# Kernel optimization log

Hardware: AMD Instinct MI355X
Metric: run time of the kernel (lower is better)

Reference implementation:

```python
import jax, jax.numpy as jnp
import numpy as np

B, C, W, H, K = 8, 512, 64, 64, 64
C4 = C // 4

def setup_inputs() -> dict:
    key = jax.random.key(0)
    ks = jax.random.split(key, 12)
    return {
        "x1": jax.random.normal(ks[0], (B, C, W, H), jnp.float32),
        "y1": jax.random.normal(ks[1], (B, K, C), jnp.float32),
        "x2": jax.random.normal(ks[2], (B, C, W, H), jnp.float32),
        "y2": jax.random.normal(ks[3], (B, K, C), jnp.float32),
        "wq": jax.random.normal(ks[4], (C4, C), jnp.float32) * 0.02,
        "bq": jax.random.normal(ks[5], (C4,), jnp.float32) * 0.02,
        "wk": jax.random.normal(ks[6], (C4, C), jnp.float32) * 0.02,
        "bk": jax.random.normal(ks[7], (C4,), jnp.float32) * 0.02,
        "wv": jax.random.normal(ks[8], (C, C), jnp.float32) * 0.02,
        "bv": jax.random.normal(ks[9], (C,), jnp.float32) * 0.02,
        "scale": jax.random.normal(ks[10], (1,), jnp.float32),
        "scale1": jax.random.normal(ks[11], (1,), jnp.float32),
    }

def reference(x1, y1, x2, y2, wq, bq, wk, bk, wv, bv, scale, scale1):
    b, c, w, h = x1.shape
    k = y1.shape[1]
    n = w * h
    # value projections (nn.Linear: y @ W^T + b), kept as [B, C, K]
    pv1 = jnp.einsum('bkc,dc->bdk', y1, wv) + bv[None, :, None]
    pv2 = jnp.einsum('bkc,dc->bdk', y2, wv) + bv[None, :, None]
    # 1x1 conv query: [B, C4, W, H] -> [B, N, C4]
    q = jnp.einsum('bcwh,dc->bwhd', x2, wq) + bq
    q = q.reshape(b, n, -1)
    # key: [B, K, C4] -> bmm contracts over C4
    kk = jnp.einsum('bkc,dc->bkd', y2, wk) + bk  # [B, K, C4]
    energy = jnp.einsum('bnd,bkd->bnk', q, kk)   # [B, N, K]
    attention = jax.nn.softmax(jnp.abs(energy), axis=-1)
    # out = value [B,C,K] @ attention^T [B,K,N] -> [B,C,N]
    out1 = jnp.einsum('bck,bnk->bcn', pv1, attention).reshape(b, c, w, h)
    out1 = scale[0] * out1 + x1
    out2 = jnp.einsum('bck,bnk->bcn', pv2, attention).reshape(b, c, w, h)
    out2 = scale1[0] * out2 + x2
    return (out1, out2)
```

## Files before the change

### kernel.cpp

```cpp
#include <hip/hip_runtime.h>
#include <math.h>

#define Bn 8
#define Cn 512
#define Kn 64
#define C4n 128
#define Nn 4096

typedef short bf16x8 __attribute__((ext_vector_type(8)));
typedef float f32x4  __attribute__((ext_vector_type(4)));
typedef unsigned short u16;

__device__ __forceinline__ u16 f2bf(float f) {
    union { float f; unsigned u; } v; v.f = f;
    unsigned r = v.u + 0x7FFF + ((v.u >> 16) & 1);
    return (u16)(r >> 16);
}
__device__ __forceinline__ float bf2f(u16 h) {
    union { unsigned u; float f; } v; v.u = ((unsigned)h) << 16;
    return v.f;
}
__device__ __forceinline__ bf16x8 cvt8(const float* p) {
    float4 a = *(const float4*)p;
    float4 b = *(const float4*)(p + 4);
    bf16x8 r;
    r[0] = (short)f2bf(a.x); r[1] = (short)f2bf(a.y);
    r[2] = (short)f2bf(a.z); r[3] = (short)f2bf(a.w);
    r[4] = (short)f2bf(b.x); r[5] = (short)f2bf(b.y);
    r[6] = (short)f2bf(b.z); r[7] = (short)f2bf(b.w);
    return r;
}

__global__ __launch_bounds__(256) void kk_pv_kernel(
    const float* __restrict__ y1, const float* __restrict__ y2,
    const float* __restrict__ wv, const float* __restrict__ bv,
    const float* __restrict__ wk, const float* __restrict__ bk,
    u16* __restrict__ pv1h, u16* __restrict__ pv2h, u16* __restrict__ kkh)
{
    const int b    = blockIdx.y;
    const int sel  = blockIdx.z;
    const int lane = threadIdx.x & 63;
    const int wid  = threadIdx.x >> 6;
    const int lr   = lane & 15;
    const int lg   = lane >> 4;

    if (sel < 2) {
        const int cb   = blockIdx.x * 64 + wid * 16;
        const float* y = sel ? y2 : y1;
        u16* pvh       = sel ? pv2h : pv1h;

        f32x4 acc[4];
        #pragma unroll
        for (int kt = 0; kt < 4; ++kt) acc[kt] = (f32x4){0.f, 0.f, 0.f, 0.f};

        for (int c0 = 0; c0 < Cn; c0 += 32) {
            const int cf = c0 + lg * 8;
            bf16x8 wfr = cvt8(wv + (size_t)(cb + lr) * Cn + cf);
            bf16x8 yfr[4];
            #pragma unroll
            for (int kt = 0; kt < 4; ++kt)
                yfr[kt] = cvt8(y + (size_t)(b * Kn + kt * 16 + lr) * Cn + cf);
            #pragma unroll
            for (int kt = 0; kt < 4; ++kt)
                acc[kt] = __builtin_amdgcn_mfma_f32_16x16x32_bf16(
                    yfr[kt], wfr, acc[kt], 0, 0, 0);
        }
        const int c = cb + lr;
        const float bb = bv[c];
        #pragma unroll
        for (int kt = 0; kt < 4; ++kt) {
            ushort4 o;
            o.x = f2bf(acc[kt][0] + bb); o.y = f2bf(acc[kt][1] + bb);
            o.z = f2bf(acc[kt][2] + bb); o.w = f2bf(acc[kt][3] + bb);
            *(ushort4*)&pvh[(((size_t)(b * Cn + c)) << 6) + kt * 16 + 4 * lg] = o;
        }
    } else {
        const int dblk = blockIdx.x * 16;
        f32x4 acc = (f32x4){0.f, 0.f, 0.f, 0.f};
        for (int c0 = 0; c0 < Cn; c0 += 32) {
            const int cf = c0 + lg * 8;
            bf16x8 wfr = cvt8(wk + (size_t)(dblk + lr) * Cn + cf);
            bf16x8 yfr = cvt8(y2 + (size_t)(b * Kn + wid * 16 + lr) * Cn + cf);
            acc = __builtin_amdgcn_mfma_f32_16x16x32_bf16(wfr, yfr, acc, 0, 0, 0);
        }
        const int d4 = dblk + 4 * lg;
        float4 bkv = *(const float4*)&bk[d4];
        ushort4 o;
        o.x = f2bf(acc[0] + bkv.x); o.y = f2bf(acc[1] + bkv.y);
        o.z = f2bf(acc[2] + bkv.z); o.w = f2bf(acc[3] + bkv.w);
        *(ushort4*)&kkh[(((size_t)(b * Kn + wid * 16 + lr)) << 7) + d4] = o;
    }
}

__global__ __launch_bounds__(256) void M_e0_kernel(
    const u16* __restrict__ kkh, const float* __restrict__ wq,
    const float* __restrict__ bq, u16* __restrict__ Mth,
    float* __restrict__ e0)
{
    const int b = blockIdx.y;
    const int t = threadIdx.x;

    if (blockIdx.x == 4) {
        if (t < Kn) {
            const u16* row = kkh + (((size_t)(b * Kn + t)) << 7);
            float acc = 0.f;
            #pragma unroll
            for (int d8 = 0; d8 < C4n; d8 += 8) {
                bf16x8 v = *(const bf16x8*)(row + d8);
                #pragma unroll
                for (int j = 0; j < 8; ++j)
                    acc += bq[d8 + j] * bf2f((u16)v[j]);
            }
            e0[b * Kn + t] = acc;
        }
        return;
    }

    const int cb   = blockIdx.x * 128 + (t >> 6) * 32;
    const int lane = t & 63;
    const int lr   = lane & 15;
    const int lg   = lane >> 4;

    f32x4 acc[2][4];
    #pragma unroll
    for (int ct = 0; ct < 2; ++ct)
        #pragma unroll
        for (int kt = 0; kt < 4; ++kt) acc[ct][kt] = (f32x4){0.f, 0.f, 0.f, 0.f};

    for (int d0 = 0; d0 < C4n; d0 += 32) {
        const int df = d0 + lg * 8;
        bf16x8 afr[2];
        #pragma unroll
        for (int ct = 0; ct < 2; ++ct) {
            const int c = cb + ct * 16 + lr;
            bf16x8 r;
            #pragma unroll
            for (int j = 0; j < 8; ++j)
                r[j] = (short)f2bf(wq[(size_t)(df + j) * Cn + c]);
            afr[ct] = r;
        }
        bf16x8 bfr[4];
        #pragma unroll
        for (int kt = 0; kt < 4; ++kt)
            bfr[kt] = *(const bf16x8*)&kkh[(((size_t)(b * Kn + kt * 16 + lr)) << 7) + df];
        #pragma unroll
        for (int ct = 0; ct < 2; ++ct)
            #pragma unroll
            for (int kt = 0; kt < 4; ++kt)
                acc[ct][kt] = __builtin_amdgcn_mfma_f32_16x16x32_bf16(
                    afr[ct], bfr[kt], acc[ct][kt], 0, 0, 0);
    }
    #pragma unroll
    for (int ct = 0; ct < 2; ++ct) {
        const int c4 = cb + ct * 16 + 4 * lg;
        #pragma unroll
        for (int kt = 0; kt < 4; ++kt) {
            ushort4 o;
            o.x = f2bf(acc[ct][kt][0]); o.y = f2bf(acc[ct][kt][1]);
            o.z = f2bf(acc[ct][kt][2]); o.w = f2bf(acc[ct][kt][3]);
            *(ushort4*)&Mth[(size_t)(b * Kn + kt * 16 + lr) * Cn + c4] = o;
        }
    }
}

__global__ __launch_bounds__(256) void energy_softmax_kernel(
    const float* __restrict__ x2, const u16* __restrict__ Mth,
    const float* __restrict__ e0, u16* __restrict__ attG)
{
    const int id   = blockIdx.x;
    const int b    = id & 7;
    const int n0   = (id >> 3) * 64;
    const int t    = threadIdx.x;
    const int lane = t & 63;
    const int wid  = t >> 6;
    const int lr   = lane & 15;
    const int lg   = lane >> 4;
    const int n    = n0 + wid * 16 + lr;

    f32x4 eacc[4];
    #pragma unroll
    for (int kt = 0; kt < 4; ++kt) eacc[kt] = (f32x4){0.f, 0.f, 0.f, 0.f};

    const float* xcol = x2 + (((size_t)b * Cn) << 12) + n;
    const u16*   mb   = Mth + ((size_t)b << 15) + (size_t)lr * Cn;

    for (int c0 = 0; c0 < Cn; c0 += 32) {
        const int cf = c0 + lg * 8;
        float xs[8];
        #pragma unroll
        for (int j = 0; j < 8; ++j)
            xs[j] = xcol[((size_t)(cf + j)) << 12];
        bf16x8 xfr;
        #pragma unroll
        for (int j = 0; j < 8; ++j) xfr[j] = (short)f2bf(xs[j]);
        #pragma unroll
        for (int kt = 0; kt < 4; ++kt) {
            bf16x8 av = *(const bf16x8*)(mb + ((size_t)kt << 13) + cf);
            eacc[kt] = __builtin_amdgcn_mfma_f32_16x16x32_bf16(av, xfr, eacc[kt], 0, 0, 0);
        }
    }

    float a[4][4];
    float mx = 0.f;
    #pragma unroll
    for (int kt = 0; kt < 4; ++kt) {
        float4 e0v = *(const float4*)&e0[b * Kn + kt * 16 + lg * 4];
        float er[4] = {e0v.x, e0v.y, e0v.z, e0v.w};
        #pragma unroll
        for (int reg = 0; reg < 4; ++reg) {
            float v = fabsf(eacc[kt][reg] + er[reg]);
            a[kt][reg] = v;
            mx = fmaxf(mx, v);
        }
    }
    mx = fmaxf(mx, __shfl_xor(mx, 16));
    mx = fmaxf(mx, __shfl_xor(mx, 32));
    float s = 0.f;
    #pragma unroll
    for (int kt = 0; kt < 4; ++kt)
        #pragma unroll
        for (int reg = 0; reg < 4; ++reg) {
            a[kt][reg] = __expf(a[kt][reg] - mx);
            s += a[kt][reg];
        }
    s += __shfl_xor(s, 16);
    s += __shfl_xor(s, 32);
    const float inv = 1.0f / s;

    u16* dst = attG + (((size_t)b << 18) + ((size_t)n << 6));
    #pragma unroll
    for (int kt = 0; kt < 4; ++kt) {
        ushort4 o;
        o.x = f2bf(a[kt][0] * inv); o.y = f2bf(a[kt][1] * inv);
        o.z = f2bf(a[kt][2] * inv); o.w = f2bf(a[kt][3] * inv);
        *(ushort4*)&dst[kt * 16 + 4 * lg] = o;
    }
}

__global__ __launch_bounds__(256) void out_kernel(
    const float* __restrict__ x1, const float* __restrict__ x2,
    const u16* __restrict__ pv1h, const u16* __restrict__ pv2h,
    const u16* __restrict__ attG,
    const float* __restrict__ scale, const float* __restrict__ scale1,
    float* __restrict__ out1, float* __restrict__ out2)
{
    __shared__ float T[64 * 68];

    const int n0   = blockIdx.x * 64;
    const int cB   = blockIdx.y * 128;
    const int b    = blockIdx.z;
    const int t    = threadIdx.x;
    const int lane = t & 63;
    const int wid  = t >> 6;
    const int lr   = lane & 15;
    const int lg   = lane >> 4;

    bf16x8 af[4][2];
    #pragma unroll
    for (int nt = 0; nt < 4; ++nt) {
        const u16* ab = attG + (((size_t)b << 18) | ((size_t)(n0 + nt * 16 + lr) << 6)) + lg * 8;
        af[nt][0] = *(const bf16x8*)ab;
        af[nt][1] = *(const bf16x8*)(ab + 32);
    }

    const float sA = scale[0], sB = scale1[0];
    const int er  = t >> 4;
    const int ech = (t & 15) * 4;

    for (int ct = 0; ct < 2; ++ct) {
        const int wc = cB + ct * 64 + wid * 16;

        const u16* p1 = pv1h + (((size_t)(b * Cn + wc + lr)) << 6) + lg * 8;
        const u16* p2 = pv2h + (((size_t)(b * Cn + wc + lr)) << 6) + lg * 8;
        bf16x8 v1[2], v2[2];
        v1[0] = *(const bf16x8*)p1;  v1[1] = *(const bf16x8*)(p1 + 32);
        v2[0] = *(const bf16x8*)p2;  v2[1] = *(const bf16x8*)(p2 + 32);

        f32x4 acc1[4], acc2[4];
        #pragma unroll
        for (int nt = 0; nt < 4; ++nt) {
            f32x4 z = (f32x4){0.f, 0.f, 0.f, 0.f};
            acc1[nt] = __builtin_amdgcn_mfma_f32_16x16x32_bf16(af[nt][0], v1[0], z, 0, 0, 0);
            acc1[nt] = __builtin_amdgcn_mfma_f32_16x16x32_bf16(af[nt][1], v1[1], acc1[nt], 0, 0, 0);
            acc2[nt] = __builtin_amdgcn_mfma_f32_16x16x32_bf16(af[nt][0], v2[0], z, 0, 0, 0);
            acc2[nt] = __builtin_amdgcn_mfma_f32_16x16x32_bf16(af[nt][1], v2[1], acc2[nt], 0, 0, 0);
        }

        __syncthreads();
        #pragma unroll
        for (int nt = 0; nt < 4; ++nt) {
            float4 v;
            v.x = acc1[nt][0]; v.y = acc1[nt][1];
            v.z = acc1[nt][2]; v.w = acc1[nt][3];
            *(float4*)&T[(wid * 16 + lr) * 68 + nt * 16 + 4 * lg] = v;
        }
        __syncthreads();
        #pragma unroll
        for (int pass = 0; pass < 4; ++pass) {
            const int rl = pass * 16 + er;
            const size_t row = (((size_t)(b * Cn + cB + ct * 64 + rl)) << 12) + n0 + ech;
            float4 a = *(const float4*)&T[rl * 68 + ech];
            float4 xv = *(const float4*)&x1[row];
            f32x4 o;
            o[0] = sA * a.x + xv.x;  o[1] = sA * a.y + xv.y;
            o[2] = sA * a.z + xv.z;  o[3] = sA * a.w + xv.w;
            __builtin_nontemporal_store(o, (f32x4*)&out1[row]);
        }

        __syncthreads();
        #pragma unroll
        for (int nt = 0; nt < 4; ++nt) {
            float4 v;
            v.x = acc2[nt][0]; v.y = acc2[nt][1];
            v.z = acc2[nt][2]; v.w = acc2[nt][3];
            *(float4*)&T[(wid * 16 + lr) * 68 + nt * 16 + 4 * lg] = v;
        }
        __syncthreads();
        #pragma unroll
        for (int pass = 0; pass < 4; ++pass) {
            const int rl = pass * 16 + er;
            const size_t row = (((size_t)(b * Cn + cB + ct * 64 + rl)) << 12) + n0 + ech;
            float4 a = *(const float4*)&T[rl * 68 + ech];
            float4 xv = *(const float4*)&x2[row];
            f32x4 o;
            o[0] = sB * a.x + xv.x;  o[1] = sB * a.y + xv.y;
            o[2] = sB * a.z + xv.z;  o[3] = sB * a.w + xv.w;
            __builtin_nontemporal_store(o, (f32x4*)&out2[row]);
        }
    }
}

extern "C" void kernel_launch(void* const* d_in, const int* in_sizes, int n_in,
                              void* d_out, int out_size, void* d_ws, size_t ws_size,
                              hipStream_t stream)
{
    const float* x1     = (const float*)d_in[0];
    const float* y1     = (const float*)d_in[1];
    const float* x2     = (const float*)d_in[2];
    const float* y2     = (const float*)d_in[3];
    const float* wq     = (const float*)d_in[4];
    const float* bq     = (const float*)d_in[5];
    const float* wk     = (const float*)d_in[6];
    const float* bk     = (const float*)d_in[7];
    const float* wv     = (const float*)d_in[8];
    const float* bv     = (const float*)d_in[9];
    const float* scale  = (const float*)d_in[10];
    const float* scale1 = (const float*)d_in[11];

    float* out1 = (float*)d_out;
    float* out2 = out1 + (size_t)Bn * Cn * Nn;

    float* ws   = (float*)d_ws;
    float* e0   = ws;
    u16*   kkh  = (u16*)(ws + 512);
    u16*   Mth  = kkh + 65536;
    u16*   pv1h = Mth + 262144;
    u16*   pv2h = pv1h + 262144;
    u16*   attG = pv2h + 262144;

    kk_pv_kernel<<<dim3(8, Bn, 3), 256, 0, stream>>>(
        y1, y2, wv, bv, wk, bk, pv1h, pv2h, kkh);
    M_e0_kernel<<<dim3(5, Bn), 256, 0, stream>>>(kkh, wq, bq, Mth, e0);
    energy_softmax_kernel<<<512, 256, 0, stream>>>(x2, Mth, e0, attG);
    out_kernel<<<dim3(64, 4, 8), 256, 0, stream>>>(
        x1, x2, pv1h, pv2h, attG, scale, scale1, out1, out2);
}
```

Measured before the change: 92.55 us.

## Fuse energy-softmax and output kernels, keeping attention in shared memory

```diff
diff --git a/kernel.cpp b/kernel.cpp
--- a/kernel.cpp
+++ b/kernel.cpp
@@ -163,10 +163,16 @@
     }
 }
 
-__global__ __launch_bounds__(256) void energy_softmax_kernel(
-    const float* __restrict__ x2, const u16* __restrict__ Mth,
-    const float* __restrict__ e0, u16* __restrict__ attG)
+__global__ __launch_bounds__(256) void attn_out_kernel(
+    const float* __restrict__ x1, const float* __restrict__ x2,
+    const u16* __restrict__ pv1h, const u16* __restrict__ pv2h,
+    const u16* __restrict__ Mth, const float* __restrict__ e0,
+    const float* __restrict__ scale, const float* __restrict__ scale1,
+    float* __restrict__ out1, float* __restrict__ out2)
 {
+    __shared__ u16   attL[64 * 64];
+    __shared__ float T[4][16 * 68];
+
     const int id   = blockIdx.x;
     const int b    = id & 7;
     const int n0   = (id >> 3) * 64;
@@ -175,13 +181,13 @@
     const int wid  = t >> 6;
     const int lr   = lane & 15;
     const int lg   = lane >> 4;
-    const int n    = n0 + wid * 16 + lr;
+    const int nl   = wid * 16 + lr;
 
     f32x4 eacc[4];
     #pragma unroll
     for (int kt = 0; kt < 4; ++kt) eacc[kt] = (f32x4){0.f, 0.f, 0.f, 0.f};
 
-    const float* xcol = x2 + (((size_t)b * Cn) << 12) + n;
+    const float* xcol = x2 + (((size_t)b * Cn) << 12) + n0 + nl;
     const u16*   mb   = Mth + ((size_t)b << 15) + (size_t)lr * Cn;
 
     for (int c0 = 0; c0 < Cn; c0 += 32) {
@@ -200,75 +206,60 @@
         }
     }
 
-    float a[4][4];
-    float mx = 0.f;
-    #pragma unroll
-    for (int kt = 0; kt < 4; ++kt) {
-        float4 e0v = *(const float4*)&e0[b * Kn + kt * 16 + lg * 4];
-        float er[4] = {e0v.x, e0v.y, e0v.z, e0v.w};
-        #pragma unroll
-        for (int reg = 0; reg < 4; ++reg) {
-            float v = fabsf(eacc[kt][reg] + er[reg]);
-            a[kt][reg] = v;
-            mx = fmaxf(mx, v);
-        }
-    }
-    mx = fmaxf(mx, __shfl_xor(mx, 16));
-    mx = fmaxf(mx, __shfl_xor(mx, 32));
-    float s = 0.f;
-    #pragma unroll
-    for (int kt = 0; kt < 4; ++kt)
-        #pragma unroll
-        for (int reg = 0; reg < 4; ++reg) {
-            a[kt][reg] = __expf(a[kt][reg] - mx);
-            s += a[kt][reg];
-        }
-    s += __shfl_xor(s, 16);
-    s += __shfl_xor(s, 32);
-    const float inv = 1.0f / s;
-
-    u16* dst = attG + (((size_t)b << 18) + ((size_t)n << 6));
-    #pragma unroll
-    for (int kt = 0; kt < 4; ++kt) {
-        ushort4 o;
-        o.x = f2bf(a[kt][0] * inv); o.y = f2bf(a[kt][1] * inv);
-        o.z = f2bf(a[kt][2] * inv); o.w = f2bf(a[kt][3] * inv);
-        *(ushort4*)&dst[kt * 16 + 4 * lg] = o;
-    }
-}
-
-__global__ __launch_bounds__(256) void out_kernel(
-    const float* __restrict__ x1, const float* __restrict__ x2,
-    const u16* __restrict__ pv1h, const u16* __restrict__ pv2h,
-    const u16* __restrict__ attG,
-    const float* __restrict__ scale, const float* __restrict__ scale1,
-    float* __restrict__ out1, float* __restrict__ out2)
-{
-    __shared__ float T[64 * 68];
-
-    const int n0   = blockIdx.x * 64;
-    const int cB   = blockIdx.y * 128;
-    const int b    = blockIdx.z;
-    const int t    = threadIdx.x;
-    const int lane = t & 63;
-    const int wid  = t >> 6;
-    const int lr   = lane & 15;
-    const int lg   = lane >> 4;
+    {
+        float a[4][4];
+        float mx = 0.f;
+        #pragma unroll
+        for (int kt = 0; kt < 4; ++kt) {
+            float4 e0v = *(const float4*)&e0[b * Kn + kt * 16 + lg * 4];
+            float er[4] = {e0v.x, e0v.y, e0v.z, e0v.w};
+            #pragma unroll
+            for (int reg = 0; reg < 4; ++reg) {
+                float v = fabsf(eacc[kt][reg] + er[reg]);
+                a[kt][reg] = v;
+                mx = fmaxf(mx, v);
+            }
+        }
+        mx = fmaxf(mx, __shfl_xor(mx, 16));
+        mx = fmaxf(mx, __shfl_xor(mx, 32));
+        float s = 0.f;
+        #pragma unroll
+        for (int kt = 0; kt < 4; ++kt)
+            #pragma unroll
+            for (int reg = 0; reg < 4; ++reg) {
+                a[kt][reg] = __expf(a[kt][reg] - mx);
+                s += a[kt][reg];
+            }
+        s += __shfl_xor(s, 16);
+        s += __shfl_xor(s, 32);
+        const float inv = 1.0f / s;
+
+        #pragma unroll
+        for (int kt = 0; kt < 4; ++kt) {
+            ushort4 o;
+            o.x = f2bf(a[kt][0] * inv); o.y = f2bf(a[kt][1] * inv);
+            o.z = f2bf(a[kt][2] * inv); o.w = f2bf(a[kt][3] * inv);
+            const int chunk = (kt * 2 + (lg >> 1)) ^ (nl & 7);
+            *(ushort4*)&attL[nl * 64 + chunk * 8 + 4 * (lg & 1)] = o;
+        }
+    }
+    __syncthreads();
 
     bf16x8 af[4][2];
     #pragma unroll
-    for (int nt = 0; nt < 4; ++nt) {
-        const u16* ab = attG + (((size_t)b << 18) | ((size_t)(n0 + nt * 16 + lr) << 6)) + lg * 8;
-        af[nt][0] = *(const bf16x8*)ab;
-        af[nt][1] = *(const bf16x8*)(ab + 32);
-    }
+    for (int nt = 0; nt < 4; ++nt)
+        #pragma unroll
+        for (int ks = 0; ks < 2; ++ks) {
+            const int nn = nt * 16 + lr;
+            const int chunk = (ks * 4 + lg) ^ (nn & 7);
+            af[nt][ks] = *(const bf16x8*)&attL[nn * 64 + chunk * 8];
+        }
 
     const float sA = scale[0], sB = scale1[0];
-    const int er  = t >> 4;
-    const int ech = (t & 15) * 4;
-
-    for (int ct = 0; ct < 2; ++ct) {
-        const int wc = cB + ct * 64 + wid * 16;
+    float* Tw = &T[wid][0];
+
+    for (int ct = 0; ct < 8; ++ct) {
+        const int wc = ct * 64 + wid * 16;
 
         const u16* p1 = pv1h + (((size_t)(b * Cn + wc + lr)) << 6) + lg * 8;
         const u16* p2 = pv2h + (((size_t)(b * Cn + wc + lr)) << 6) + lg * 8;
@@ -286,20 +277,18 @@
             acc2[nt] = __builtin_amdgcn_mfma_f32_16x16x32_bf16(af[nt][1], v2[1], acc2[nt], 0, 0, 0);
         }
 
-        __syncthreads();
         #pragma unroll
         for (int nt = 0; nt < 4; ++nt) {
             float4 v;
             v.x = acc1[nt][0]; v.y = acc1[nt][1];
             v.z = acc1[nt][2]; v.w = acc1[nt][3];
-            *(float4*)&T[(wid * 16 + lr) * 68 + nt * 16 + 4 * lg] = v;
-        }
-        __syncthreads();
-        #pragma unroll
-        for (int pass = 0; pass < 4; ++pass) {
-            const int rl = pass * 16 + er;
-            const size_t row = (((size_t)(b * Cn + cB + ct * 64 + rl)) << 12) + n0 + ech;
-            float4 a = *(const float4*)&T[rl * 68 + ech];
+            *(float4*)&Tw[lr * 68 + nt * 16 + 4 * lg] = v;
+        }
+        #pragma unroll
+        for (int r4 = 0; r4 < 4; ++r4) {
+            const int rloc = r4 * 4 + lg;
+            const size_t row = (((size_t)(b * Cn + wc + rloc)) << 12) + n0 + lr * 4;
+            float4 a = *(const float4*)&Tw[rloc * 68 + lr * 4];
             float4 xv = *(const float4*)&x1[row];
             f32x4 o;
             o[0] = sA * a.x + xv.x;  o[1] = sA * a.y + xv.y;
@@ -307,20 +296,18 @@
             __builtin_nontemporal_store(o, (f32x4*)&out1[row]);
         }
 
-        __syncthreads();
         #pragma unroll
         for (int nt = 0; nt < 4; ++nt) {
             float4 v;
             v.x = acc2[nt][0]; v.y = acc2[nt][1];
             v.z = acc2[nt][2]; v.w = acc2[nt][3];
-            *(float4*)&T[(wid * 16 + lr) * 68 + nt * 16 + 4 * lg] = v;
-        }
-        __syncthreads();
-        #pragma unroll
-        for (int pass = 0; pass < 4; ++pass) {
-            const int rl = pass * 16 + er;
-            const size_t row = (((size_t)(b * Cn + cB + ct * 64 + rl)) << 12) + n0 + ech;
-            float4 a = *(const float4*)&T[rl * 68 + ech];
+            *(float4*)&Tw[lr * 68 + nt * 16 + 4 * lg] = v;
+        }
+        #pragma unroll
+        for (int r4 = 0; r4 < 4; ++r4) {
+            const int rloc = r4 * 4 + lg;
+            const size_t row = (((size_t)(b * Cn + wc + rloc)) << 12) + n0 + lr * 4;
+            float4 a = *(const float4*)&Tw[rloc * 68 + lr * 4];
             float4 xv = *(const float4*)&x2[row];
             f32x4 o;
             o[0] = sB * a.x + xv.x;  o[1] = sB * a.y + xv.y;
@@ -356,12 +343,10 @@
     u16*   Mth  = kkh + 65536;
     u16*   pv1h = Mth + 262144;
     u16*   pv2h = pv1h + 262144;
-    u16*   attG = pv2h + 262144;
 
     kk_pv_kernel<<<dim3(8, Bn, 3), 256, 0, stream>>>(
         y1, y2, wv, bv, wk, bk, pv1h, pv2h, kkh);
     M_e0_kernel<<<dim3(5, Bn), 256, 0, stream>>>(kkh, wq, bq, Mth, e0);
-    energy_softmax_kernel<<<512, 256, 0, stream>>>(x2, Mth, e0, attG);
-    out_kernel<<<dim3(64, 4, 8), 256, 0, stream>>>(
-        x1, x2, pv1h, pv2h, attG, scale, scale1, out1, out2);
-}
+    attn_out_kernel<<<512, 256, 0, stream>>>(
+        x1, x2, pv1h, pv2h, Mth, e0, scale, scale1, out1, out2);
+}
```

Result: faster. 86.04 us (-7.0%).
